# Optimization experiments

Hardware: AMD Instinct MI355X
Metric: run time of the kernel (lower is better)

The kernel has to match this reference:

```python
import jax, jax.numpy as jnp
import numpy as np

EPS = 0.1           # entropic regularization epsilon
MAX_ITER = 100
THRESH = 0.1        # early-stop threshold on mean |u - u_prev|
LOG_EPS = 1e-8


def setup_inputs() -> dict:
    key = jax.random.key(0)
    kx, ky = jax.random.split(key)
    x = jax.random.normal(kx, (8, 1024, 3), dtype=jnp.float32)
    y = jax.random.normal(ky, (8, 1024, 3), dtype=jnp.float32)
    return {"x": x, "y": y}


def _sqdist(x, y):
    # squared euclidean cost matrix [B, N, N]  (== torch.cdist(x,y,p=2)**2)
    x2 = jnp.sum(x * x, axis=-1)[:, :, None]
    y2 = jnp.sum(y * y, axis=-1)[:, None, :]
    xy = jnp.einsum("bnd,bmd->bnm", x, y)
    return jnp.maximum(x2 + y2 - 2.0 * xy, 0.0)


def reference(x, y):
    B, N, D = x.shape
    C = _sqdist(x, y)                      # [B, N, N]
    log_mu = jnp.log(1.0 / N + LOG_EPS)    # scalar (uniform marginals)
    log_nu = log_mu

    u0 = jnp.zeros((B, N), dtype=x.dtype)
    v0 = jnp.zeros((B, N), dtype=x.dtype)

    def step(carry, _):
        u, v, done = carry
        # u-update uses old v
        M1 = (u[:, :, None] + v[:, None, :] - C) / EPS          # [B,N,N]
        u_new = EPS * (log_mu - jax.nn.logsumexp(M1, axis=-1)) + u
        # v-update uses new u
        M2 = (u_new[:, :, None] + v[:, None, :] - C) / EPS
        v_new = EPS * (log_nu - jax.nn.logsumexp(M2, axis=-2)) + v
        # freeze once converged (mimics torch early break)
        u_out = jnp.where(done, u, u_new)
        v_out = jnp.where(done, v, v_new)
        err = jnp.mean(jnp.abs(u_out - u))
        done_new = done | (err < THRESH)
        return (u_out, v_out, done_new), None

    (u, v, _), _ = jax.lax.scan(step, (u0, v0, jnp.array(False)), None, length=MAX_ITER)

    PI = jnp.exp((u[:, :, None] + v[:, None, :] - C) / EPS)     # transport plan
    emd = jnp.sum(PI * C, axis=(-2, -1))                        # [B]
    return jnp.mean(emd)                                        # reduction='mean'
```

## Files before the change

### kernel.cpp

```cpp
#include <hip/hip_runtime.h>

typedef unsigned int uint_t;
typedef unsigned long long u64_t;

constexpr int B = 8;
constexpr int N = 1024;
constexpr int NBLOCKS = 256;
constexpr int NTHREADS = 512;
constexpr int NWAVES = NTHREADS / 64;
constexpr int BPB = NBLOCKS / B;
constexpr int SEG = N / BPB;
constexpr int RPW = SEG / NWAVES;
constexpr int KPL = N / 64;
constexpr int MAX_ITER = 100;
constexpr float THRESH = 0.1f;
constexpr float K2 = 14.42695040888963f;
constexpr float A2K = 2.0f * K2;
constexpr float NEPSLN2 = -0.06931471805599453f;
constexpr float EPSLOGMU = -0.693146156565634f;
constexpr uint_t MAGIC = 0xC0FFEE01u;

constexpr int OFF_U    = 0;
constexpr int OFF_V    = OFF_U + B * N;
constexpr int OFF_ZERO = OFF_V + B * N;
constexpr int OFF_FLGA = OFF_ZERO;
constexpr int OFF_FLGB = OFF_FLGA + 512;
constexpr int OFF_ERRB = OFF_FLGB + 512;
constexpr int OFF_EMD  = OFF_ERRB + 64;
constexpr int OFF_ZEROEND = OFF_EMD + 16;
constexpr int OFF_INIT = OFF_ZEROEND;

__device__ __forceinline__ float gload(const float* p) {
  return __hip_atomic_load(p, __ATOMIC_RELAXED, __HIP_MEMORY_SCOPE_AGENT);
}
__device__ __forceinline__ void gstore(float* p, float v) {
  __hip_atomic_store(p, v, __ATOMIC_RELAXED, __HIP_MEMORY_SCOPE_AGENT);
}
__device__ __forceinline__ uint_t l32(const uint_t* p) {
  return __hip_atomic_load(p, __ATOMIC_RELAXED, __HIP_MEMORY_SCOPE_AGENT);
}
__device__ __forceinline__ void s32(uint_t* p, uint_t v) {
  __hip_atomic_store(p, v, __ATOMIC_RELAXED, __HIP_MEMORY_SCOPE_AGENT);
}
__device__ __forceinline__ u64_t l64(const u64_t* p) {
  return __hip_atomic_load(p, __ATOMIC_RELAXED, __HIP_MEMORY_SCOPE_AGENT);
}
__device__ __forceinline__ void s64(u64_t* p, u64_t v) {
  __hip_atomic_store(p, v, __ATOMIC_RELAXED, __HIP_MEMORY_SCOPE_AGENT);
}
__device__ __forceinline__ void drain() { __builtin_amdgcn_s_waitcnt(0); }

__device__ __forceinline__ u64_t pk64(uint_t tag, float v) {
  return ((u64_t)tag << 32) | (u64_t)__float_as_uint(v);
}

__device__ __forceinline__ float wsum(float v) {
#pragma unroll
  for (int o = 32; o; o >>= 1) v += __shfl_xor(v, o);
  return v;
}
__device__ __forceinline__ float wmax(float v) {
#pragma unroll
  for (int o = 32; o; o >>= 1) v = fmaxf(v, __shfl_xor(v, o));
  return v;
}

__device__ __forceinline__ float block_sum(float v, float* sh) {
  v = wsum(v);
  const int wave = threadIdx.x >> 6;
  const int lane = threadIdx.x & 63;
  if (lane == 0) sh[wave] = v;
  __syncthreads();
  float tot = 0.f;
#pragma unroll
  for (int w = 0; w < NWAVES; ++w) tot += sh[w];
  __syncthreads();
  return tot;
}

template <bool TRACK>
__device__ __forceinline__ float half_compute(
    const float* __restrict__ cx, const float* __restrict__ cy,
    const float* __restrict__ cz, const float* __restrict__ cw,
    const float* __restrict__ rx, const float* __restrict__ ry,
    const float* __restrict__ rz, const float* __restrict__ rw,
    const float* __restrict__ pin, const float* __restrict__ pout_old,
    float (&pnew)[RPW], int i0, int lane, bool pin_zero, bool first_out) {
  float p2[KPL];
#pragma unroll
  for (int k = 0; k < KPL; ++k)
    p2[k] = pin_zero ? 0.f : gload(&pin[lane + (k << 6)]) * K2;

  float a0[RPW], a1[RPW], a2[RPW], X[RPW], m[RPW];
  float vals[RPW][KPL];
#pragma unroll
  for (int rr = 0; rr < RPW; ++rr) {
    a0[rr] = A2K * rx[i0 + rr]; a1[rr] = A2K * ry[i0 + rr];
    a2[rr] = A2K * rz[i0 + rr];
    X[rr] = -rw[i0 + rr];
    m[rr] = -3.4e38f;
  }
#pragma unroll
  for (int k = 0; k < KPL; ++k) {
    const int j = lane + (k << 6);
    float ccx = cx[j], ccy = cy[j], ccz = cz[j];
    float base = cw[j] + p2[k];
#pragma unroll
    for (int rr = 0; rr < RPW; ++rr) {
      float t = fmaf(a0[rr], ccx, fmaf(a1[rr], ccy, fmaf(a2[rr], ccz, base)));
      float val = fminf(t - X[rr], p2[k]);
      vals[rr][k] = val;
      m[rr] = fmaxf(m[rr], val);
    }
  }
  float err = 0.f;
#pragma unroll
  for (int rr = 0; rr < RPW; ++rr) {
    float mr = wmax(m[rr]);
    float s = 0.f;
#pragma unroll
    for (int k = 0; k < KPL; ++k)
      s += __builtin_amdgcn_exp2f(vals[rr][k] - mr);
    s = wsum(s);
    float pn = fmaf(NEPSLN2, mr + __builtin_amdgcn_logf(s), EPSLOGMU);
    pnew[rr] = pn;
    if (TRACK && lane == 0) {
      float old = first_out ? 0.f : gload(&pout_old[i0 + rr]);
      err += fabsf(pn - old);
    }
  }
  return err;
}

__device__ __forceinline__ void store_rows(float* p, const float (&pnew)[RPW],
                                           int i0, int lane) {
  if (lane == 0) {
#pragma unroll
    for (int rr = 0; rr < RPW; ++rr) gstore(&p[i0 + rr], pnew[rr]);
  }
}

__global__ void __launch_bounds__(NTHREADS, 2) sinkhorn_kernel(
    const float* __restrict__ xg, const float* __restrict__ yg,
    float* __restrict__ out, float* __restrict__ ws) {
  __shared__ float s_xx[N], s_xy[N], s_xz[N], s_xw[N];
  __shared__ float s_yx[N], s_yy[N], s_yz[N], s_yw[N];
  __shared__ float sh_red[NWAVES];

  const int bid = blockIdx.x;
  const int tid = threadIdx.x;
  const int b = bid & 7;
  const int seg = bid >> 3;
  const int wave = tid >> 6;
  const int lane = tid & 63;
  const int i0 = seg * SEG + wave * RPW;

  float* u = ws + OFF_U + b * N;
  float* v = ws + OFF_V + b * N;
  u64_t* flgA = (u64_t*)(ws + OFF_FLGA) + b * 32;
  u64_t* flgB = (u64_t*)(ws + OFF_FLGB) + b * 32;
  u64_t* errB = (u64_t*)(ws + OFF_ERRB);
  u64_t* emdB = (u64_t*)(ws + OFF_EMD);
  uint_t* init_flag = (uint_t*)(ws + OFF_INIT);

  if (bid == 0) {
    u64_t* zb = (u64_t*)(ws + OFF_ZERO);
    for (int i = tid; i < (OFF_ZEROEND - OFF_ZERO) / 2; i += NTHREADS)
      s64(&zb[i], 0ull);
    drain();
    __syncthreads();
    if (tid == 0) s32(init_flag, MAGIC);
  }

  for (int p = tid; p < N; p += NTHREADS) {
    const float* xp = xg + (size_t)(b * N + p) * 3;
    float x0 = xp[0], x1 = xp[1], x2 = xp[2];
    s_xx[p] = x0; s_xy[p] = x1; s_xz[p] = x2;
    s_xw[p] = -K2 * (x0 * x0 + x1 * x1 + x2 * x2);
    const float* yp = yg + (size_t)(b * N + p) * 3;
    float y0 = yp[0], y1 = yp[1], y2 = yp[2];
    s_yx[p] = y0; s_yy[p] = y1; s_yz[p] = y2;
    s_yw[p] = -K2 * (y0 * y0 + y1 * y1 + y2 * y2);
  }
  __syncthreads();

  float un[RPW];
  float my_err = half_compute<true>(s_yx, s_yy, s_yz, s_yw,
                                    s_xx, s_xy, s_xz, s_xw,
                                    v, u, un, i0, lane,
                                    true, true);
  store_rows(u, un, i0, lane);
  drain();
  float blk_err = block_sum(my_err, sh_red);
  if (tid == 0 && bid != 0)
    while (l32(init_flag) != MAGIC) __builtin_amdgcn_s_sleep(2);
  __syncthreads();
  if (tid == 0) s64(&flgA[seg], pk64(1u, blk_err));

  int it = 0;
  for (;;) {
    const uint_t want = (uint_t)(it + 1);

    if (wave == 0) {
      float pay;
      for (;;) {
        u64_t pk = (lane < BPB) ? l64(&flgA[lane]) : ~0ull;
        if (__all((uint_t)(pk >> 32) >= want)) { pay = __uint_as_float((uint_t)pk); break; }
        __builtin_amdgcn_s_sleep(1);
      }
      if (seg == 0) {
        float e = wsum((lane < BPB) ? pay : 0.f);
        if (lane == 0) s64(&errB[(it & 3) * 8 + b], pk64(want, e));
      }
    }
    __syncthreads();

    float vn[RPW];
    half_compute<false>(s_xx, s_xy, s_xz, s_xw,
                        s_yx, s_yy, s_yz, s_yw,
                        u, nullptr, vn, i0, lane, false, false);
    store_rows(v, vn, i0, lane);
    drain();
    __syncthreads();
    if (tid == 0) s64(&flgB[seg], pk64(want, 0.f));

    if (wave == 0) {
      for (;;) {
        u64_t pk = (lane < BPB) ? l64(&flgB[lane]) : ~0ull;
        if (__all((uint_t)(pk >> 32) >= want)) break;
        __builtin_amdgcn_s_sleep(1);
      }
    }
    __syncthreads();

    if (it == MAX_ITER - 1) break;

    my_err = half_compute<true>(s_yx, s_yy, s_yz, s_yw,
                                s_xx, s_xy, s_xz, s_xw,
                                v, u, un, i0, lane, false, false);

    if (wave == 0) {
      float pay;
      for (;;) {
        u64_t pk = (lane < B) ? l64(&errB[(it & 3) * 8 + lane]) : ~0ull;
        if (__all((uint_t)(pk >> 32) >= want)) { pay = __uint_as_float((uint_t)pk); break; }
        __builtin_amdgcn_s_sleep(1);
      }
      float e = wsum((lane < B) ? pay : 0.f);
      if (lane == 0) sh_red[0] = e;
    }
    __syncthreads();
    float tot = sh_red[0];
    __syncthreads();
    if (tot * (1.f / (B * N)) < THRESH) break;

    store_rows(u, un, i0, lane);
    drain();
    blk_err = block_sum(my_err, sh_red);
    if (tid == 0) s64(&flgA[seg], pk64((uint_t)(it + 2), blk_err));
    ++it;
  }

  float p2e[KPL];
#pragma unroll
  for (int k = 0; k < KPL; ++k) p2e[k] = gload(&v[lane + (k << 6)]) * K2;
  float acc = 0.f;
#pragma unroll
  for (int rr = 0; rr < RPW; ++rr) {
    const int i = i0 + rr;
    float a0 = A2K * s_xx[i], a1 = A2K * s_xy[i], a2 = A2K * s_xz[i];
    float X = -s_xw[i];
    float u2 = gload(&u[i]) * K2;
#pragma unroll
    for (int k = 0; k < KPL; ++k) {
      const int j = lane + (k << 6);
      float t = fmaf(a0, s_yx[j], fmaf(a1, s_yy[j], fmaf(a2, s_yz[j], s_yw[j])));
      float kc = fmaxf(X - t, 0.f);
      acc = fmaf(__builtin_amdgcn_exp2f(u2 + p2e[k] - kc), kc, acc);
    }
  }
  float blk = block_sum(acc, sh_red);
  const uint_t ef = (uint_t)(it + 2);
  if (tid == 0) s64(&flgB[seg], pk64(ef, blk));

  if (seg == 0 && wave == 0) {
    float pay;
    for (;;) {
      u64_t pk = (lane < BPB) ? l64(&flgB[lane]) : ~0ull;
      if (__all((uint_t)(pk >> 32) >= ef)) { pay = __uint_as_float((uint_t)pk); break; }
      __builtin_amdgcn_s_sleep(1);
    }
    float e = wsum((lane < BPB) ? pay : 0.f);
    if (lane == 0) s64(&emdB[b], pk64(1u, e));
  }
  if (bid == 0 && wave == 0) {
    float pay;
    for (;;) {
      u64_t pk = (lane < B) ? l64(&emdB[lane]) : ~0ull;
      if (__all((uint_t)(pk >> 32) >= 1u)) { pay = __uint_as_float((uint_t)pk); break; }
      __builtin_amdgcn_s_sleep(1);
    }
    float e = wsum((lane < B) ? pay : 0.f);
    if (lane == 0) out[0] = e * (1.f / (B * K2));
  }
}

extern "C" void kernel_launch(void* const* d_in, const int* in_sizes, int n_in,
                              void* d_out, int out_size, void* d_ws, size_t ws_size,
                              hipStream_t stream) {
  const float* x = (const float*)d_in[0];
  const float* y = (const float*)d_in[1];
  float* out = (float*)d_out;
  float* ws = (float*)d_ws;
  void* args[] = { (void*)&x, (void*)&y, (void*)&out, (void*)&ws };
  hipLaunchCooperativeKernel((const void*)sinkhorn_kernel,
                             dim3(NBLOCKS), dim3(NTHREADS), args, 0, stream);
}
```

Before: 110.3 us.

## Overlap convergence check with next u-update and pack point data as float2

```diff
diff --git a/kernel.cpp b/kernel.cpp
--- a/kernel.cpp
+++ b/kernel.cpp
@@ -26,8 +26,7 @@
 constexpr int OFF_FLGA = OFF_ZERO;
 constexpr int OFF_FLGB = OFF_FLGA + 512;
 constexpr int OFF_ERRB = OFF_FLGB + 512;
-constexpr int OFF_EMD  = OFF_ERRB + 64;
-constexpr int OFF_ZEROEND = OFF_EMD + 16;
+constexpr int OFF_ZEROEND = OFF_ERRB + 64;
 constexpr int OFF_INIT = OFF_ZEROEND;
 
 __device__ __forceinline__ float gload(const float* p) {
@@ -78,36 +77,34 @@
   return tot;
 }
 
-template <bool TRACK>
+template <bool TRACK, bool PIN_ZERO>
 __device__ __forceinline__ float half_compute(
-    const float* __restrict__ cx, const float* __restrict__ cy,
-    const float* __restrict__ cz, const float* __restrict__ cw,
-    const float* __restrict__ rx, const float* __restrict__ ry,
-    const float* __restrict__ rz, const float* __restrict__ rw,
-    const float* __restrict__ pin, const float* __restrict__ pout_old,
-    float (&pnew)[RPW], int i0, int lane, bool pin_zero, bool first_out) {
+    const float2* __restrict__ cxy, const float2* __restrict__ czw,
+    const float2* __restrict__ rxy, const float2* __restrict__ rzw,
+    const float* __restrict__ pin, float* __restrict__ pout,
+    const float (&prev)[RPW], float (&pnew)[RPW], int i0, int lane) {
   float p2[KPL];
 #pragma unroll
   for (int k = 0; k < KPL; ++k)
-    p2[k] = pin_zero ? 0.f : gload(&pin[lane + (k << 6)]) * K2;
+    p2[k] = PIN_ZERO ? 0.f : gload(&pin[lane + (k << 6)]) * K2;
 
   float a0[RPW], a1[RPW], a2[RPW], X[RPW], m[RPW];
   float vals[RPW][KPL];
 #pragma unroll
   for (int rr = 0; rr < RPW; ++rr) {
-    a0[rr] = A2K * rx[i0 + rr]; a1[rr] = A2K * ry[i0 + rr];
-    a2[rr] = A2K * rz[i0 + rr];
-    X[rr] = -rw[i0 + rr];
+    float2 rA = rxy[i0 + rr], rB = rzw[i0 + rr];
+    a0[rr] = A2K * rA.x; a1[rr] = A2K * rA.y; a2[rr] = A2K * rB.x;
+    X[rr] = -rB.y;
     m[rr] = -3.4e38f;
   }
 #pragma unroll
   for (int k = 0; k < KPL; ++k) {
     const int j = lane + (k << 6);
-    float ccx = cx[j], ccy = cy[j], ccz = cz[j];
-    float base = cw[j] + p2[k];
+    float2 cA = cxy[j], cB = czw[j];
+    float base = cB.y + p2[k];
 #pragma unroll
     for (int rr = 0; rr < RPW; ++rr) {
-      float t = fmaf(a0[rr], ccx, fmaf(a1[rr], ccy, fmaf(a2[rr], ccz, base)));
+      float t = fmaf(a0[rr], cA.x, fmaf(a1[rr], cA.y, fmaf(a2[rr], cB.x, base)));
       float val = fminf(t - X[rr], p2[k]);
       vals[rr][k] = val;
       m[rr] = fmaxf(m[rr], val);
@@ -124,27 +121,19 @@
     s = wsum(s);
     float pn = fmaf(NEPSLN2, mr + __builtin_amdgcn_logf(s), EPSLOGMU);
     pnew[rr] = pn;
-    if (TRACK && lane == 0) {
-      float old = first_out ? 0.f : gload(&pout_old[i0 + rr]);
-      err += fabsf(pn - old);
+    if (lane == 0) {
+      gstore(&pout[i0 + rr], pn);
+      if (TRACK) err += fabsf(pn - prev[rr]);
     }
   }
   return err;
-}
-
-__device__ __forceinline__ void store_rows(float* p, const float (&pnew)[RPW],
-                                           int i0, int lane) {
-  if (lane == 0) {
-#pragma unroll
-    for (int rr = 0; rr < RPW; ++rr) gstore(&p[i0 + rr], pnew[rr]);
-  }
 }
 
 __global__ void __launch_bounds__(NTHREADS, 2) sinkhorn_kernel(
     const float* __restrict__ xg, const float* __restrict__ yg,
     float* __restrict__ out, float* __restrict__ ws) {
-  __shared__ float s_xx[N], s_xy[N], s_xz[N], s_xw[N];
-  __shared__ float s_yx[N], s_yy[N], s_yz[N], s_yw[N];
+  __shared__ float2 s_xxy[N], s_xzw[N];
+  __shared__ float2 s_yxy[N], s_yzw[N];
   __shared__ float sh_red[NWAVES];
 
   const int bid = blockIdx.x;
@@ -159,8 +148,8 @@
   float* v = ws + OFF_V + b * N;
   u64_t* flgA = (u64_t*)(ws + OFF_FLGA) + b * 32;
   u64_t* flgB = (u64_t*)(ws + OFF_FLGB) + b * 32;
+  u64_t* flgB_all = (u64_t*)(ws + OFF_FLGB);
   u64_t* errB = (u64_t*)(ws + OFF_ERRB);
-  u64_t* emdB = (u64_t*)(ws + OFF_EMD);
   uint_t* init_flag = (uint_t*)(ws + OFF_INIT);
 
   if (bid == 0) {
@@ -172,32 +161,43 @@
     if (tid == 0) s32(init_flag, MAGIC);
   }
 
-  for (int p = tid; p < N; p += NTHREADS) {
-    const float* xp = xg + (size_t)(b * N + p) * 3;
-    float x0 = xp[0], x1 = xp[1], x2 = xp[2];
-    s_xx[p] = x0; s_xy[p] = x1; s_xz[p] = x2;
-    s_xw[p] = -K2 * (x0 * x0 + x1 * x1 + x2 * x2);
-    const float* yp = yg + (size_t)(b * N + p) * 3;
-    float y0 = yp[0], y1 = yp[1], y2 = yp[2];
-    s_yx[p] = y0; s_yy[p] = y1; s_yz[p] = y2;
-    s_yw[p] = -K2 * (y0 * y0 + y1 * y1 + y2 * y2);
+  {
+    const float2* xp = (const float2*)(xg + (size_t)b * N * 3) + 3 * tid;
+    float2 g0 = xp[0], g1 = xp[1], g2 = xp[2];
+    s_xxy[2 * tid]     = g0;
+    s_xzw[2 * tid]     = make_float2(g1.x, -K2 * (g0.x * g0.x + g0.y * g0.y + g1.x * g1.x));
+    s_xxy[2 * tid + 1] = make_float2(g1.y, g2.x);
+    s_xzw[2 * tid + 1] = make_float2(g2.y, -K2 * (g1.y * g1.y + g2.x * g2.x + g2.y * g2.y));
+    const float2* yp = (const float2*)(yg + (size_t)b * N * 3) + 3 * tid;
+    float2 h0 = yp[0], h1 = yp[1], h2 = yp[2];
+    s_yxy[2 * tid]     = h0;
+    s_yzw[2 * tid]     = make_float2(h1.x, -K2 * (h0.x * h0.x + h0.y * h0.y + h1.x * h1.x));
+    s_yxy[2 * tid + 1] = make_float2(h1.y, h2.x);
+    s_yzw[2 * tid + 1] = make_float2(h2.y, -K2 * (h1.y * h1.y + h2.x * h2.x + h2.y * h2.y));
   }
   __syncthreads();
 
-  float un[RPW];
-  float my_err = half_compute<true>(s_yx, s_yy, s_yz, s_yw,
-                                    s_xx, s_xy, s_xz, s_xw,
-                                    v, u, un, i0, lane,
-                                    true, true);
-  store_rows(u, un, i0, lane);
+  float un[RPW], un_prev[RPW];
+#pragma unroll
+  for (int rr = 0; rr < RPW; ++rr) un_prev[rr] = 0.f;
+  float my_err = half_compute<true, true>(s_yxy, s_yzw, s_xxy, s_xzw,
+                                          v, u, un_prev, un, i0, lane);
   drain();
-  float blk_err = block_sum(my_err, sh_red);
+  float werr = wsum(my_err);
+  if (lane == 0) sh_red[wave] = werr;
   if (tid == 0 && bid != 0)
     while (l32(init_flag) != MAGIC) __builtin_amdgcn_s_sleep(2);
   __syncthreads();
-  if (tid == 0) s64(&flgA[seg], pk64(1u, blk_err));
+  if (tid == 0) {
+    float e = 0.f;
+#pragma unroll
+    for (int w = 0; w < NWAVES; ++w) e += sh_red[w];
+    s64(&flgA[seg], pk64(1u, e));
+  }
 
   int it = 0;
+  int final_it;
+  bool use_prev;
   for (;;) {
     const uint_t want = (uint_t)(it + 1);
 
@@ -215,11 +215,9 @@
     }
     __syncthreads();
 
-    float vn[RPW];
-    half_compute<false>(s_xx, s_xy, s_xz, s_xw,
-                        s_yx, s_yy, s_yz, s_yw,
-                        u, nullptr, vn, i0, lane, false, false);
-    store_rows(v, vn, i0, lane);
+    float vn[RPW], vdummy[RPW];
+    half_compute<false, false>(s_xxy, s_xzw, s_yxy, s_yzw,
+                               u, v, vdummy, vn, i0, lane);
     drain();
     __syncthreads();
     if (tid == 0) s64(&flgB[seg], pk64(want, 0.f));
@@ -233,31 +231,38 @@
     }
     __syncthreads();
 
-    if (it == MAX_ITER - 1) break;
-
-    my_err = half_compute<true>(s_yx, s_yy, s_yz, s_yw,
-                                s_xx, s_xy, s_xz, s_xw,
-                                v, u, un, i0, lane, false, false);
-
-    if (wave == 0) {
-      float pay;
-      for (;;) {
-        u64_t pk = (lane < B) ? l64(&errB[(it & 3) * 8 + lane]) : ~0ull;
-        if (__all((uint_t)(pk >> 32) >= want)) { pay = __uint_as_float((uint_t)pk); break; }
-        __builtin_amdgcn_s_sleep(1);
-      }
-      float e = wsum((lane < B) ? pay : 0.f);
-      if (lane == 0) sh_red[0] = e;
-    }
-    __syncthreads();
-    float tot = sh_red[0];
-    __syncthreads();
-    if (tot * (1.f / (B * N)) < THRESH) break;
-
-    store_rows(u, un, i0, lane);
+    if (it == MAX_ITER - 1) { final_it = it + 1; use_prev = false; break; }
+
+    u64_t dpre = (lane < B) ? l64(&errB[(it & 3) * 8 + lane]) : ~0ull;
+
+#pragma unroll
+    for (int rr = 0; rr < RPW; ++rr) un_prev[rr] = un[rr];
+    my_err = half_compute<true, false>(s_yxy, s_yzw, s_xxy, s_xzw,
+                                       v, u, un_prev, un, i0, lane);
     drain();
-    blk_err = block_sum(my_err, sh_red);
-    if (tid == 0) s64(&flgA[seg], pk64((uint_t)(it + 2), blk_err));
+    werr = wsum(my_err);
+    if (lane == 0) sh_red[wave] = werr;
+    __syncthreads();
+    if (tid == 0) {
+      float e = 0.f;
+#pragma unroll
+      for (int w = 0; w < NWAVES; ++w) e += sh_red[w];
+      s64(&flgA[seg], pk64((uint_t)(it + 2), e));
+    }
+
+    float tot;
+    for (;;) {
+      if (__all((uint_t)(dpre >> 32) >= want)) {
+        tot = wsum((lane < B) ? __uint_as_float((uint_t)dpre) : 0.f);
+        break;
+      }
+      __builtin_amdgcn_s_sleep(1);
+      dpre = (lane < B) ? l64(&errB[(it & 3) * 8 + lane]) : ~0ull;
+    }
+    if (tot * (1.f / (B * N)) < THRESH) {
+      final_it = it + 1; use_prev = true;
+      break;
+    }
     ++it;
   }
 
@@ -268,40 +273,36 @@
 #pragma unroll
   for (int rr = 0; rr < RPW; ++rr) {
     const int i = i0 + rr;
-    float a0 = A2K * s_xx[i], a1 = A2K * s_xy[i], a2 = A2K * s_xz[i];
-    float X = -s_xw[i];
-    float u2 = gload(&u[i]) * K2;
+    float2 rA = s_xxy[i], rB = s_xzw[i];
+    float a0 = A2K * rA.x, a1 = A2K * rA.y, a2 = A2K * rB.x;
+    float X = -rB.y;
+    float u2 = (use_prev ? un_prev[rr] : un[rr]) * K2;
 #pragma unroll
     for (int k = 0; k < KPL; ++k) {
       const int j = lane + (k << 6);
-      float t = fmaf(a0, s_yx[j], fmaf(a1, s_yy[j], fmaf(a2, s_yz[j], s_yw[j])));
+      float2 cA = s_yxy[j], cB = s_yzw[j];
+      float t = fmaf(a0, cA.x, fmaf(a1, cA.y, fmaf(a2, cB.x, cB.y)));
       float kc = fmaxf(X - t, 0.f);
       acc = fmaf(__builtin_amdgcn_exp2f(u2 + p2e[k] - kc), kc, acc);
     }
   }
   float blk = block_sum(acc, sh_red);
-  const uint_t ef = (uint_t)(it + 2);
+  const uint_t ef = (uint_t)(final_it + 1);
   if (tid == 0) s64(&flgB[seg], pk64(ef, blk));
 
-  if (seg == 0 && wave == 0) {
-    float pay;
-    for (;;) {
-      u64_t pk = (lane < BPB) ? l64(&flgB[lane]) : ~0ull;
-      if (__all((uint_t)(pk >> 32) >= ef)) { pay = __uint_as_float((uint_t)pk); break; }
-      __builtin_amdgcn_s_sleep(1);
-    }
-    float e = wsum((lane < BPB) ? pay : 0.f);
-    if (lane == 0) s64(&emdB[b], pk64(1u, e));
-  }
-  if (bid == 0 && wave == 0) {
-    float pay;
-    for (;;) {
-      u64_t pk = (lane < B) ? l64(&emdB[lane]) : ~0ull;
-      if (__all((uint_t)(pk >> 32) >= 1u)) { pay = __uint_as_float((uint_t)pk); break; }
-      __builtin_amdgcn_s_sleep(1);
-    }
-    float e = wsum((lane < B) ? pay : 0.f);
-    if (lane == 0) out[0] = e * (1.f / (B * K2));
+  if (bid == 0) {
+    float part = 0.f;
+    if (wave < 4) {
+      u64_t pk;
+      for (;;) {
+        pk = l64(&flgB_all[(wave << 6) + lane]);
+        if (__all((uint_t)(pk >> 32) >= ef)) break;
+        __builtin_amdgcn_s_sleep(1);
+      }
+      part = __uint_as_float((uint_t)pk);
+    }
+    float tot = block_sum(part, sh_red);
+    if (tid == 0) out[0] = tot * (1.f / (B * K2));
   }
 }
 
```

Measured after the change: 107.5 us. -2.5%, faster.
